# Kernel tuning notes

Measured on AMD Instinct MI355X. Metric: run time of the kernel, lower is better.

Reference implementation:

```python
import jax, jax.numpy as jnp
import numpy as np

N = 2048   # num nodes
D = 512    # hidden_dim


def setup_inputs() -> dict:
    key = jax.random.key(0)
    k1, k2 = jax.random.split(key)
    x = jax.random.normal(k1, (N, D), dtype=jnp.float32)
    # linear: hidden_dim -> 1 (xavier-like scale)
    w = jax.random.normal(k2, (D,), dtype=jnp.float32) * (1.0 / np.sqrt(D))
    b = jnp.zeros((1,), dtype=jnp.float32)
    return {"x": x, "w": w, "b": b}


def reference(x, w, b):
    # euclidean_distance_matrix + linear fused:
    # s[i,j] = sum_d w_d * (x[i,d]-x[j,d])^2 + b
    #        = q_i + q_j - 2*(x*w) @ x^T + b,  q_i = sum_d w_d x[i,d]^2
    xw = x * w                              # [N, D]
    q = jnp.sum(xw * x, axis=1)             # [N]
    cross = xw @ x.T                        # [N, N]
    s = q[:, None] + q[None, :] - 2.0 * cross + b[0]
    grouping_matrix = jax.nn.sigmoid(s)     # [N, N]

    # compute_fielder, similarity_graph='base'
    W = grouping_matrix
    degree = jnp.sum(W, axis=1)
    L = jnp.diag(degree) - W                # symmetric graph Laplacian
    eigen_values, eigen_vectors = jnp.linalg.eigh(L)
    order = jnp.argsort(jnp.abs(eigen_values))
    fielder_value = eigen_values[order[1]]
    fielder_vector = eigen_vectors[:, order[1]]
    return grouping_matrix, fielder_value, fielder_vector
```

## Files before the change

### kernel.cpp

```cpp
#include <hip/hip_runtime.h>
#include <math.h>

constexpr int NN = 2048;
constexpr int DD_ = 512;
constexpr int LM = 64;
constexpr int VS = NN + 32;
constexpr int GPART = 8;
constexpr int MVB = 512;
#define SIGN_FLIP 1


typedef __attribute__((ext_vector_type(4))) float f32x4;
typedef __attribute__((ext_vector_type(8))) short bf16x8;

__device__ inline double waveReduceSum(double v) {
#pragma unroll
  for (int off = 32; off; off >>= 1) v += __shfl_down(v, off, 64);
  return v;
}

__device__ inline double blockReduceSum256(double v) {
  __shared__ double sm[4];
  int lane = threadIdx.x & 63;
  int wid  = threadIdx.x >> 6;
  v = waveReduceSum(v);
  __syncthreads();
  if (lane == 0) sm[wid] = v;
  __syncthreads();
  double r = 0.0;
  if (threadIdx.x < 4) r = sm[threadIdx.x];
  if (wid == 0) {
    r += __shfl_down(r, 2, 64);
    r += __shfl_down(r, 1, 64);
  }
  return r;
}

__device__ inline double blockReduceSum128(double v) {
  __shared__ double sm[2];
  int lane = threadIdx.x & 63;
  int wid  = threadIdx.x >> 6;
  v = waveReduceSum(v);
  if (lane == 0) sm[wid] = v;
  __syncthreads();
  double r = 0.0;
  if (threadIdx.x == 0) r = sm[0] + sm[1];
  return r;
}

__device__ inline unsigned short f2bf(float f) {
  unsigned u = __float_as_uint(f);
  u += 0x7FFFu + ((u >> 16) & 1u);
  return (unsigned short)(u >> 16);
}
__device__ inline float bf2f(unsigned short h) {
  return __uint_as_float(((unsigned)h) << 16);
}

__global__ __launch_bounds__(128) void k_cvtq(const float* __restrict__ x,
                                              const float* __restrict__ w,
                                              float* __restrict__ q,
                                              unsigned short* __restrict__ ah,
                                              unsigned short* __restrict__ al,
                                              unsigned short* __restrict__ bh,
                                              unsigned short* __restrict__ bl) {
  int row = blockIdx.x, t = threadIdx.x;
  int d = 4 * t;
  float4 xv = *(const float4*)&x[(size_t)row * DD_ + d];
  float4 wv = *(const float4*)&w[d];
  float xs[4] = {xv.x, xv.y, xv.z, xv.w};
  float wsv[4] = {wv.x, wv.y, wv.z, wv.w};
  unsigned short rah[4], ral[4], rbh[4], rbl[4];
  float accq = 0.f;
#pragma unroll
  for (int kq = 0; kq < 4; ++kq) {
    float xf = xs[kq], wf = wsv[kq];
    float a = xf * wf;
    unsigned short h = f2bf(a);
    rah[kq] = h;
    ral[kq] = f2bf(a - bf2f(h));
    unsigned short hb = f2bf(xf);
    rbh[kq] = hb;
    rbl[kq] = f2bf(xf - bf2f(hb));
    accq += wf * xf * xf;
  }
  ushort4 vA = {rah[0], rah[1], rah[2], rah[3]};
  ushort4 vAl = {ral[0], ral[1], ral[2], ral[3]};
  ushort4 vB = {rbh[0], rbh[1], rbh[2], rbh[3]};
  ushort4 vBl = {rbl[0], rbl[1], rbl[2], rbl[3]};
  *(ushort4*)&ah[(size_t)row * DD_ + d] = vA;
  *(ushort4*)&al[(size_t)row * DD_ + d] = vAl;
  *(ushort4*)&bh[(size_t)row * DD_ + d] = vB;
  *(ushort4*)&bl[(size_t)row * DD_ + d] = vBl;
  double rq = blockReduceSum128((double)accq);
  if (t == 0) q[row] = (float)rq;
}

__global__ __launch_bounds__(256) void k_Wm(const unsigned short* __restrict__ ah,
                                            const unsigned short* __restrict__ al,
                                            const unsigned short* __restrict__ bh,
                                            const unsigned short* __restrict__ bl,
                                            const float* __restrict__ q,
                                            const float* __restrict__ bptr,
                                            float* __restrict__ out) {
  const int bx = blockIdx.x, by = blockIdx.y;
  if (bx < by) return;
  union SmemU {
    struct { unsigned short As[2][128][40]; unsigned short Bs[2][128][40]; } ab;
    float tr[64][132];
  };
  __shared__ SmemU sm;
  const int t = threadIdx.x;
  const int i0 = by * 128, j0 = bx * 128;
  const int lane = t & 63, wv = t >> 6;
  const int wr = wv >> 1, wc = wv & 1;
  const int fr = lane & 15, kc = lane >> 4;
  const int srow = t >> 1, scol = (t & 1) * 16;

  f32x4 acc[4][4];
#pragma unroll
  for (int a = 0; a < 4; ++a)
#pragma unroll
    for (int b = 0; b < 4; ++b) acc[a][b] = (f32x4){0.f, 0.f, 0.f, 0.f};

  {
    bf16x8 ra0 = *(const bf16x8*)&ah[(size_t)(i0 + srow) * DD_ + scol];
    bf16x8 ra1 = *(const bf16x8*)&ah[(size_t)(i0 + srow) * DD_ + scol + 8];
    bf16x8 rb0 = *(const bf16x8*)&bh[(size_t)(j0 + srow) * DD_ + scol];
    bf16x8 rb1 = *(const bf16x8*)&bh[(size_t)(j0 + srow) * DD_ + scol + 8];
    *(bf16x8*)&sm.ab.As[0][srow][scol] = ra0;
    *(bf16x8*)&sm.ab.As[0][srow][scol + 8] = ra1;
    *(bf16x8*)&sm.ab.Bs[0][srow][scol] = rb0;
    *(bf16x8*)&sm.ab.Bs[0][srow][scol + 8] = rb1;
  }
  __syncthreads();
  int cur = 0;
  for (int s = 0; s < 48; ++s) {
    bf16x8 na0, na1, nb0, nb1;
    if (s + 1 < 48) {
      int pass = (s + 1) >> 4;
      int kk = ((s + 1) & 15) * 32;
      const unsigned short* srcA = (pass == 2) ? al : ah;
      const unsigned short* srcB = (pass == 1) ? bl : bh;
      na0 = *(const bf16x8*)&srcA[(size_t)(i0 + srow) * DD_ + kk + scol];
      na1 = *(const bf16x8*)&srcA[(size_t)(i0 + srow) * DD_ + kk + scol + 8];
      nb0 = *(const bf16x8*)&srcB[(size_t)(j0 + srow) * DD_ + kk + scol];
      nb1 = *(const bf16x8*)&srcB[(size_t)(j0 + srow) * DD_ + kk + scol + 8];
    }
    bf16x8 af[4], bq[4];
#pragma unroll
    for (int a = 0; a < 4; ++a)
      af[a] = *(const bf16x8*)&sm.ab.As[cur][wr * 64 + a * 16 + fr][kc * 8];
#pragma unroll
    for (int b = 0; b < 4; ++b)
      bq[b] = *(const bf16x8*)&sm.ab.Bs[cur][wc * 64 + b * 16 + fr][kc * 8];
#pragma unroll
    for (int a = 0; a < 4; ++a)
#pragma unroll
      for (int b = 0; b < 4; ++b)
        acc[a][b] = __builtin_amdgcn_mfma_f32_16x16x32_bf16(af[a], bq[b], acc[a][b], 0, 0, 0);
    if (s + 1 < 48) {
      *(bf16x8*)&sm.ab.As[cur ^ 1][srow][scol] = na0;
      *(bf16x8*)&sm.ab.As[cur ^ 1][srow][scol + 8] = na1;
      *(bf16x8*)&sm.ab.Bs[cur ^ 1][srow][scol] = nb0;
      *(bf16x8*)&sm.ab.Bs[cur ^ 1][srow][scol + 8] = nb1;
    }
    __syncthreads();
    cur ^= 1;
  }
  float b0 = bptr[0];
#pragma unroll
  for (int a = 0; a < 4; ++a) {
#pragma unroll
    for (int rg = 0; rg < 4; ++rg) {
      int i = i0 + wr * 64 + a * 16 + kc * 4 + rg;
      float qi = q[i];
#pragma unroll
      for (int b = 0; b < 4; ++b) {
        int j = j0 + wc * 64 + b * 16 + fr;
        float s = qi + q[j] - 2.0f * acc[a][b][rg] + b0;
        float sig = 1.0f / (1.0f + expf(-s));
        acc[a][b][rg] = sig;
        out[(size_t)i * NN + j] = sig;
      }
    }
  }
  if (bx != by) {
#pragma unroll
    for (int h = 0; h < 2; ++h) {
      __syncthreads();
      if (wc == h) {
#pragma unroll
        for (int a = 0; a < 4; ++a)
#pragma unroll
          for (int b = 0; b < 4; ++b)
            *(f32x4*)&sm.tr[b * 16 + fr][wr * 64 + a * 16 + kc * 4] = acc[a][b];
      }
      __syncthreads();
#pragma unroll
      for (int p = 0; p < 8; ++p) {
        int f = p * 256 + t;
        int rr_ = f >> 5, c4 = (f & 31) * 4;
        float4 v = *(const float4*)&sm.tr[rr_][c4];
        *(float4*)&out[(size_t)(j0 + h * 64 + rr_) * NN + i0 + c4] = v;
      }
    }
  }
}

__global__ __launch_bounds__(256) void k_init(double* __restrict__ r,
                                              double* __restrict__ part) {
  int t = threadIdx.x;
  double loc[8];
  double s = 0.0;
#pragma unroll
  for (int p = 0; p < 8; ++p) {
    unsigned i = (unsigned)(t + 256 * p);
    unsigned u = i * 2654435761u + 0x9E3779B9u;
    u ^= u >> 16; u *= 0x85EBCA6Bu; u ^= u >> 13; u *= 0xC2B2AE35u; u ^= u >> 16;
    double val = ((double)u / 4294967296.0) - 0.5;
    loc[p] = val; s += val;
  }
  __shared__ double mean_s, inv_s;
  double tot = blockReduceSum256(s);
  if (t == 0) mean_s = tot / (double)NN;
  __syncthreads();
  double mean = mean_s;
  double ss = 0.0;
#pragma unroll
  for (int p = 0; p < 8; ++p) { loc[p] -= mean; ss += loc[p] * loc[p]; }
  double tss = blockReduceSum256(ss);
  if (t == 0) inv_s = 1.0 / sqrt(tss);
  __syncthreads();
  double inv = inv_s;
#pragma unroll
  for (int p = 0; p < 8; ++p) r[t + 256 * p] = loc[p] * inv;
  if (t < GPART) part[t] = (t == 0) ? 1.0 : 0.0;
}

__global__ __launch_bounds__(256) void k_mva(const float* __restrict__ Wm,
                                             double* __restrict__ deg,
                                             const double* __restrict__ rprev,
                                             const double* __restrict__ part,
                                             double* __restrict__ V,
                                             double* __restrict__ wstash,
                                             double* __restrict__ c,
                                             double* __restrict__ beta, int j) {
  int b = blockIdx.x, t = threadIdx.x;
  double ss = 0.0;
#pragma unroll
  for (int p = 0; p < GPART; ++p) ss += part[p];
  double bet = sqrt(ss);
  double inv = (bet > 1e-3) ? 1.0 / bet : 0.0;

  if (b < MVB) {
    const int lane = t & 63, w = t >> 6;
    const int row = b * 4 + w;
    const float* wr = Wm + (size_t)row * NN;
    double acc = 0.0, dsum = 0.0;
    if (j == 0) {
#pragma unroll
      for (int p = 0; p < 8; ++p) {
        int i = 4 * lane + 256 * p;
        float4 wl = *(const float4*)&wr[i];
        dsum += (double)wl.x + (double)wl.y + (double)wl.z + (double)wl.w;
        acc += (double)wl.x * rprev[i] + (double)wl.y * rprev[i + 1] +
               (double)wl.z * rprev[i + 2] + (double)wl.w * rprev[i + 3];
      }
    } else {
#pragma unroll
      for (int p = 0; p < 8; ++p) {
        int i = 4 * lane + 256 * p;
        float4 wl = *(const float4*)&wr[i];
        acc += (double)wl.x * rprev[i] + (double)wl.y * rprev[i + 1] +
               (double)wl.z * rprev[i + 2] + (double)wl.w * rprev[i + 3];
      }
    }
    acc = waveReduceSum(acc);
    if (j == 0) dsum = waveReduceSum(dsum);
    if (lane == 0) {
      double d;
      if (j == 0) { d = dsum; deg[row] = d; }
      else d = deg[row];
      double vj = rprev[row] * inv;
      V[(size_t)j * VS + row] = vj;
      wstash[(size_t)j * VS + row] = d * vj - acc * inv;
      if (row == 0 && j > 0) beta[j - 1] = (bet > 1e-3) ? bet : 0.0;
    }
  } else {
    int q = b - MVB;
    const double* wq = wstash + (size_t)q * VS;
    double a = 0.0;
#pragma unroll
    for (int p = 0; p < 8; ++p) { int i = t + 256 * p; a += wq[i] * rprev[i]; }
    double red = blockReduceSum256(a);
    if (t == 0) c[q] = red * inv;
  }
}

__global__ __launch_bounds__(256) void k_orthb(const double* __restrict__ V,
                                               const double* __restrict__ wstash,
                                               const double* __restrict__ c,
                                               double* __restrict__ r,
                                               double* __restrict__ part,
                                               double* __restrict__ alpha, int j) {
  __shared__ double cs[LM];
  __shared__ double cj_s, s1_s;
  int b = blockIdx.x, t = threadIdx.x;
  const double* wj = wstash + (size_t)j * VS;
  const double* vj = V + (size_t)j * VS;
  double a = 0.0, s = 0.0;
#pragma unroll
  for (int p = 0; p < 8; ++p) {
    int i = t + 256 * p;
    double wv = wj[i];
    a += vj[i] * wv;
    s += wv;
  }
  double cj = blockReduceSum256(a);
  double s1 = blockReduceSum256(s);
  if (t == 0) { cj_s = cj; s1_s = s1; }
  for (int k = t; k < j; k += 256) cs[k] = c[k];
  __syncthreads();
  double cjv = cj_s, s1v = s1_s;
  int i = b * 256 + t;
  double val = wj[i] - s1v / (double)NN - cjv * vj[i];
  for (int k = 0; k < j; ++k) val -= cs[k] * V[(size_t)k * VS + i];
  r[i] = val;
  double rr = blockReduceSum256(val * val);
  if (t == 0) {
    part[b] = rr;
    if (b == 0) alpha[j] = cjv;
  }
}

__device__ inline double guardpiv(double d) {
  if (fabs(d) < 1e-280) return (d < 0.0) ? -1e-280 : 1e-280;
  return d;
}

template <int NB_>
__device__ inline int sturm_cnt(double p, double al_r, double be_r, int nn) {
  const int lim = NB_ ? NB_ : nn;
  int cnt = 0;
  double d = __shfl(al_r, 0, 64) - p;
  if (d < 0.0) cnt++;
  double ai = __shfl(al_r, 1, 64);
  double bi = __shfl(be_r, 0, 64);
  for (int i = 1; i < lim; ++i) {
    double ai_n = 0.0, bi_n = 0.0;
    if (i + 1 < lim) { ai_n = __shfl(al_r, i + 1, 64); bi_n = __shfl(be_r, i, 64); }
    if (fabs(d) < 1e-300) d = (d < 0.0) ? -1e-300 : 1e-300;
    d = (ai - p) - bi * bi / d;
    if (d < 0.0) cnt++;
    ai = ai_n; bi = bi_n;
  }
  return cnt;
}

__global__ __launch_bounds__(64) void k_tri(const double* __restrict__ alpha,
                                            const double* __restrict__ beta,
                                            double* __restrict__ svec) {
  const int t = threadIdx.x;
  double al_r = alpha[t];
  double be_r = (t < LM - 1) ? beta[t] : 0.0;

  int cand = isfinite(al_r) ? LM : t;
  int candb = (t < LM - 1 && (be_r == 0.0 || !isfinite(be_r))) ? (t + 1) : LM;
  int m = min(cand, candb);
#pragma unroll
  for (int off = 32; off; off >>= 1) m = min(m, __shfl_down(m, off, 64));
  m = __shfl(m, 0, 64);
  if (m < 2) m = 2;
  const int n = m;

  double be_prev = __shfl_up(be_r, 1, 64);
  double lo = 1e300, hi = -1e300;
  if (t < n) {
    double rr = 0.0;
    if (t > 0) rr += fabs(be_prev);
    if (t < n - 1) rr += fabs(be_r);
    lo = al_r - rr;
    hi = al_r + rr;
  }
#pragma unroll
  for (int off = 32; off; off >>= 1) {
    lo = fmin(lo, __shfl_down(lo, off, 64));
    hi = fmax(hi, __shfl_down(hi, off, 64));
  }
  lo = __shfl(lo, 0, 64);
  hi = __shfl(hi, 0, 64);

  double B0 = lo, B1 = hi;
  for (int round = 0; round < 3; ++round) {
    double p = B0 + (B1 - B0) * ((double)(t + 1) / 65.0);
    int cnt = (n == LM) ? sturm_cnt<LM>(p, al_r, be_r, n)
                        : sturm_cnt<0>(p, al_r, be_r, n);
    unsigned long long nz = __ballot(cnt > 0);
    double nl, nh;
    if (nz) {
      int first = __ffsll(nz) - 1;
      nh = B0 + (B1 - B0) * ((double)(first + 1) / 65.0);
      nl = (first > 0) ? (B0 + (B1 - B0) * ((double)first / 65.0)) : B0;
    } else {
      nl = B0 + (B1 - B0) * (64.0 / 65.0);
      nh = B1;
    }
    B0 = nl; B1 = nh;
  }
  const double sigma = 0.5 * (B0 + B1);

  double Dgf = 0.0, Dl_s = 0.0, Du_s = 0.0, Du2_s = 0.0;
  int piv_s = 0;
  {
    double dg = __shfl(al_r, 0, 64) - sigma;
    double bl = __shfl(be_r, 0, 64);
    double du = bl;
    double a1 = __shfl(al_r, 1, 64);
    double b1 = (2 < n) ? __shfl(be_r, 1, 64) : 0.0;
    for (int i = 0; i < n - 1; ++i) {
      double a1_n = 0.0, b1_n = 0.0;
      if (i + 2 < n) a1_n = __shfl(al_r, i + 2, 64);
      if (i + 3 < n) b1_n = __shfl(be_r, i + 2, 64);
      double dg_ip1 = a1 - sigma;
      double be_ip1 = b1;
      double dg_n, du_n;
      if (fabs(dg) >= fabs(bl)) {
        double fact = bl / guardpiv(dg);
        if (t == i) { Dgf = dg; Dl_s = fact; Du_s = du; Du2_s = 0.0; piv_s = 0; }
        dg_n = dg_ip1 - fact * du;
        du_n = be_ip1;
      } else {
        double fact = dg / bl;
        if (t == i) { Dgf = bl; Dl_s = fact; Du_s = dg_ip1; Du2_s = be_ip1; piv_s = 1; }
        dg_n = du - fact * dg_ip1;
        du_n = -fact * be_ip1;
      }
      dg = dg_n; du = du_n;
      bl = b1; a1 = a1_n; b1 = b1_n;
    }
    if (t == n - 1) Dgf = dg;
  }

  double bbf = 1.0;
  {
    double cur = 1.0;
    double dl = __shfl(Dl_s, 0, 64);
    int pv = __shfl(piv_s, 0, 64);
    for (int i = 0; i < n - 1; ++i) {
      double dl_n = 0.0; int pv_n = 0;
      if (i + 1 < n - 1) { dl_n = __shfl(Dl_s, i + 1, 64); pv_n = __shfl(piv_s, i + 1, 64); }
      double nxt;
      if (!pv) {
        if (t == i) bbf = cur;
        nxt = 1.0 - dl * cur;
      } else {
        if (t == i) bbf = 1.0;
        nxt = cur - dl;
      }
      cur = nxt;
      dl = dl_n; pv = pv_n;
    }
    if (t == n - 1) bbf = cur;
  }

  double xv = 0.0;
  {
    double idg = 1.0 / guardpiv(Dgf);
    double x1 = 0.0, x2 = 0.0;
    double bi = __shfl(bbf, n - 1, 64);
    double idgi = __shfl(idg, n - 1, 64);
    double dui = __shfl(Du_s, n - 1, 64);
    double du2i = __shfl(Du2_s, n - 1, 64);
    for (int i = n - 1; i >= 0; --i) {
      double bi_n = 0.0, idgi_n = 0.0, dui_n = 0.0, du2i_n = 0.0;
      if (i > 0) {
        bi_n = __shfl(bbf, i - 1, 64);
        idgi_n = __shfl(idg, i - 1, 64);
        dui_n = __shfl(Du_s, i - 1, 64);
        du2i_n = __shfl(Du2_s, i - 1, 64);
      }
      double num = bi;
      if (i < n - 1) num -= dui * x1;
      if (i < n - 2) num -= du2i * x2;
      double xi = num * idgi;
      if (t == i) xv = xi;
      x2 = x1; x1 = xi;
      bi = bi_n; idgi = idgi_n; dui = dui_n; du2i = du2i_n;
    }
  }

  double nrm = (t < n) ? xv * xv : 0.0;
#pragma unroll
  for (int off = 32; off; off >>= 1) nrm += __shfl_down(nrm, off, 64);
  nrm = __shfl(nrm, 0, 64);
  double s = 1.0 / sqrt(nrm);
  svec[t] = (t < n) ? xv * s : 0.0;
}

__global__ __launch_bounds__(256) void k_ritz(const double* __restrict__ V,
                                              const double* __restrict__ s,
                                              double* __restrict__ u) {
  __shared__ double cs[LM];
  int t = threadIdx.x;
  for (int k = t; k < LM; k += 256) cs[k] = s[k];
  __syncthreads();
  int i = blockIdx.x * 256 + t;
  double acc = 0.0;
  for (int k = 0; k < LM; ++k) acc += cs[k] * V[(size_t)k * VS + i];
  u[i] = acc;
}

__global__ __launch_bounds__(256) void k_mvu(const float* __restrict__ Wm,
                                             const double* __restrict__ deg,
                                             const double* __restrict__ v,
                                             double* __restrict__ w) {
  int row = blockIdx.x, t = threadIdx.x;
  const float* wr = Wm + (size_t)row * NN;
  double acc = 0.0;
#pragma unroll
  for (int p = 0; p < 2; ++p) {
    int i = 4 * t + 1024 * p;
    float4 wl = *(const float4*)&wr[i];
    acc += (double)wl.x * v[i] + (double)wl.y * v[i + 1] +
           (double)wl.z * v[i + 2] + (double)wl.w * v[i + 3];
  }
  double r = blockReduceSum256(acc);
  if (t == 0) w[row] = deg[row] * v[row] - r;
}

__global__ __launch_bounds__(256) void k_tail(const double* __restrict__ u,
                                              const double* __restrict__ lu,
                                              float* __restrict__ out_lam,
                                              float* __restrict__ outv) {
  __shared__ double mv[256];
  __shared__ int mi[256];
  __shared__ double mean_s, scale_s;
  int t = threadIdx.x;
  double a = 0.0, b = 0.0;
#pragma unroll
  for (int p = 0; p < 8; ++p) {
    int i = t + 256 * p;
    a += u[i] * lu[i];
    b += u[i] * u[i];
  }
  double ra = blockReduceSum256(a);
  double rb = blockReduceSum256(b);
  if (t == 0) *out_lam = (float)(ra / rb);
  double loc[8];
  double s = 0.0;
#pragma unroll
  for (int p = 0; p < 8; ++p) { loc[p] = u[t + 256 * p]; s += loc[p]; }
  double tot = blockReduceSum256(s);
  if (t == 0) mean_s = tot / (double)NN;
  __syncthreads();
  double mean = mean_s;
  double ss = 0.0, bv = -1.0;
  int bi = 0;
#pragma unroll
  for (int p = 0; p < 8; ++p) {
    loc[p] -= mean;
    ss += loc[p] * loc[p];
    double aa = fabs(loc[p]);
    if (aa > bv) { bv = aa; bi = p; }
  }
  double tss = blockReduceSum256(ss);
  mv[t] = bv; mi[t] = t + 256 * bi;
  __syncthreads();
  for (int off = 128; off; off >>= 1) {
    if (t < off) {
      if (mv[t + off] > mv[t]) { mv[t] = mv[t + off]; mi[t] = mi[t + off]; }
    }
    __syncthreads();
  }
  if (t == 0) {
    int gi = mi[0];
    double best = u[gi] - mean_s;
    double sgn = (best < 0.0) ? -1.0 : 1.0;
#if SIGN_FLIP
    sgn = -sgn;
#endif
    scale_s = sgn / sqrt(tss);
  }
  __syncthreads();
  double sc = scale_s;
#pragma unroll
  for (int p = 0; p < 8; ++p) outv[t + 256 * p] = (float)(loc[p] * sc);
}

extern "C" void kernel_launch(void* const* d_in, const int* in_sizes, int n_in,
                              void* d_out, int out_size, void* d_ws, size_t ws_size,
                              hipStream_t stream) {
  const float* x = (const float*)d_in[0];
  const float* wv = (const float*)d_in[1];
  const float* bp = (const float*)d_in[2];
  float* out = (float*)d_out;

  char* ws = (char*)d_ws;
  size_t off = 0;
  auto alloc = [&](size_t bytes) -> char* {
    char* p = ws + off;
    off = (off + bytes + 255) & ~(size_t)255;
    return p;
  };
  float* q      = (float*)alloc((size_t)NN * 4);
  double* deg   = (double*)alloc((size_t)NN * 8);
  double* r     = (double*)alloc((size_t)NN * 8);
  double* u     = (double*)alloc((size_t)NN * 8);
  double* c     = (double*)alloc((size_t)(LM + 2) * 8);
  double* alpha = (double*)alloc((size_t)LM * 8);
  double* beta  = (double*)alloc((size_t)LM * 8);
  double* svec  = (double*)alloc((size_t)LM * 8);
  double* part  = (double*)alloc((size_t)GPART * 8);
  char* un = alloc((size_t)4 * NN * DD_ * 2);
  unsigned short* ah = (unsigned short*)un;
  unsigned short* al = ah + (size_t)NN * DD_;
  unsigned short* bh = al + (size_t)NN * DD_;
  unsigned short* bl = bh + (size_t)NN * DD_;
  double* V      = (double*)un;
  double* wstash = V + (size_t)LM * VS;
  (void)ws_size; (void)in_sizes; (void)n_in; (void)out_size;

  k_cvtq<<<NN, 128, 0, stream>>>(x, wv, q, ah, al, bh, bl);
  dim3 g(NN / 128, NN / 128);
  k_Wm<<<g, 256, 0, stream>>>(ah, al, bh, bl, q, bp, out);
  k_init<<<1, 256, 0, stream>>>(r, part);

  for (int j = 0; j < LM; ++j) {
    k_mva<<<MVB + j, 256, 0, stream>>>(out, deg, r, part, V, wstash, c, beta, j);
    k_orthb<<<NN / 256, 256, 0, stream>>>(V, wstash, c, r, part, alpha, j);
  }
  k_tri<<<1, 64, 0, stream>>>(alpha, beta, svec);
  k_ritz<<<NN / 256, 256, 0, stream>>>(V, svec, u);
  k_mvu<<<NN, 256, 0, stream>>>(out, deg, u, r);
  k_tail<<<1, 256, 0, stream>>>(u, r, out + (size_t)NN * NN,
                                out + (size_t)NN * NN + 1);
}
```

Before: 810.7 us.

## Fuse Lanczos matvec and orthogonalization kernels using an atomic counter barrier

Each Lanczos step previously ran two kernels: a matvec/projection kernel and then an orthogonalization kernel. They are merged into one launch with 8 extra trailing blocks. Those blocks spin on a per-iteration atomic counter until every matvec and projection block has published its results with relaxed atomic stores and fences, then do the orthogonalization. This halves the number of launches and the inter-kernel gaps in the 64-step loop. In exchange it depends on the trailing blocks being scheduled after the producer blocks, and it adds spin-wait and fence overhead.

```diff
diff --git a/kernel.cpp b/kernel.cpp
--- a/kernel.cpp
+++ b/kernel.cpp
@@ -209,7 +209,8 @@
 }
 
 __global__ __launch_bounds__(256) void k_init(double* __restrict__ r,
-                                              double* __restrict__ part) {
+                                              double* __restrict__ part,
+                                              unsigned* __restrict__ cnt) {
   int t = threadIdx.x;
   double loc[8];
   double s = 0.0;
@@ -236,17 +237,20 @@
 #pragma unroll
   for (int p = 0; p < 8; ++p) r[t + 256 * p] = loc[p] * inv;
   if (t < GPART) part[t] = (t == 0) ? 1.0 : 0.0;
-}
-
-__global__ __launch_bounds__(256) void k_mva(const float* __restrict__ Wm,
-                                             double* __restrict__ deg,
-                                             const double* __restrict__ rprev,
-                                             const double* __restrict__ part,
-                                             double* __restrict__ V,
-                                             double* __restrict__ wstash,
-                                             double* __restrict__ c,
-                                             double* __restrict__ beta, int j) {
-  int b = blockIdx.x, t = threadIdx.x;
+  if (t < LM) cnt[t] = 0;
+}
+
+__global__ __launch_bounds__(256, 4) void k_ab(const float* __restrict__ Wm,
+                                               double* __restrict__ deg,
+                                               double* __restrict__ r,
+                                               double* __restrict__ part,
+                                               double* __restrict__ V,
+                                               double* __restrict__ wstash,
+                                               double* __restrict__ c,
+                                               double* __restrict__ alpha,
+                                               double* __restrict__ beta,
+                                               unsigned* __restrict__ cnt, int j) {
+  const int b = blockIdx.x, t = threadIdx.x;
   double ss = 0.0;
 #pragma unroll
   for (int p = 0; p < GPART; ++p) ss += part[p];
@@ -264,16 +268,16 @@
         int i = 4 * lane + 256 * p;
         float4 wl = *(const float4*)&wr[i];
         dsum += (double)wl.x + (double)wl.y + (double)wl.z + (double)wl.w;
-        acc += (double)wl.x * rprev[i] + (double)wl.y * rprev[i + 1] +
-               (double)wl.z * rprev[i + 2] + (double)wl.w * rprev[i + 3];
+        acc += (double)wl.x * r[i] + (double)wl.y * r[i + 1] +
+               (double)wl.z * r[i + 2] + (double)wl.w * r[i + 3];
       }
     } else {
 #pragma unroll
       for (int p = 0; p < 8; ++p) {
         int i = 4 * lane + 256 * p;
         float4 wl = *(const float4*)&wr[i];
-        acc += (double)wl.x * rprev[i] + (double)wl.y * rprev[i + 1] +
-               (double)wl.z * rprev[i + 2] + (double)wl.w * rprev[i + 3];
+        acc += (double)wl.x * r[i] + (double)wl.y * r[i + 1] +
+               (double)wl.z * r[i + 2] + (double)wl.w * r[i + 3];
       }
     }
     acc = waveReduceSum(acc);
@@ -282,55 +286,63 @@
       double d;
       if (j == 0) { d = dsum; deg[row] = d; }
       else d = deg[row];
-      double vj = rprev[row] * inv;
-      V[(size_t)j * VS + row] = vj;
-      wstash[(size_t)j * VS + row] = d * vj - acc * inv;
+      double vj = r[row] * inv;
+      __hip_atomic_store(&V[(size_t)j * VS + row], vj,
+                         __ATOMIC_RELAXED, __HIP_MEMORY_SCOPE_AGENT);
+      __hip_atomic_store(&wstash[(size_t)j * VS + row], d * vj - acc * inv,
+                         __ATOMIC_RELAXED, __HIP_MEMORY_SCOPE_AGENT);
       if (row == 0 && j > 0) beta[j - 1] = (bet > 1e-3) ? bet : 0.0;
     }
-  } else {
+    __syncthreads();
+    if (t == 0) { __threadfence(); atomicAdd(&cnt[j], 1u); }
+  } else if (b < MVB + j) {
     int q = b - MVB;
     const double* wq = wstash + (size_t)q * VS;
     double a = 0.0;
 #pragma unroll
-    for (int p = 0; p < 8; ++p) { int i = t + 256 * p; a += wq[i] * rprev[i]; }
+    for (int p = 0; p < 8; ++p) { int i = t + 256 * p; a += wq[i] * r[i]; }
     double red = blockReduceSum256(a);
-    if (t == 0) c[q] = red * inv;
-  }
-}
-
-__global__ __launch_bounds__(256) void k_orthb(const double* __restrict__ V,
-                                               const double* __restrict__ wstash,
-                                               const double* __restrict__ c,
-                                               double* __restrict__ r,
-                                               double* __restrict__ part,
-                                               double* __restrict__ alpha, int j) {
-  __shared__ double cs[LM];
-  __shared__ double cj_s, s1_s;
-  int b = blockIdx.x, t = threadIdx.x;
-  const double* wj = wstash + (size_t)j * VS;
-  const double* vj = V + (size_t)j * VS;
-  double a = 0.0, s = 0.0;
-#pragma unroll
-  for (int p = 0; p < 8; ++p) {
-    int i = t + 256 * p;
-    double wv = wj[i];
-    a += vj[i] * wv;
-    s += wv;
-  }
-  double cj = blockReduceSum256(a);
-  double s1 = blockReduceSum256(s);
-  if (t == 0) { cj_s = cj; s1_s = s1; }
-  for (int k = t; k < j; k += 256) cs[k] = c[k];
-  __syncthreads();
-  double cjv = cj_s, s1v = s1_s;
-  int i = b * 256 + t;
-  double val = wj[i] - s1v / (double)NN - cjv * vj[i];
-  for (int k = 0; k < j; ++k) val -= cs[k] * V[(size_t)k * VS + i];
-  r[i] = val;
-  double rr = blockReduceSum256(val * val);
-  if (t == 0) {
-    part[b] = rr;
-    if (b == 0) alpha[j] = cjv;
+    if (t == 0) {
+      __hip_atomic_store(&c[q], red * inv, __ATOMIC_RELAXED, __HIP_MEMORY_SCOPE_AGENT);
+      __threadfence();
+      atomicAdd(&cnt[j], 1u);
+    }
+  } else {
+    const int s = b - MVB - j;
+    __shared__ double cs[LM];
+    __shared__ double cj_s, s1_s;
+    if (t == 0) {
+      const unsigned tgt = (unsigned)(MVB + j);
+      while (__hip_atomic_load(&cnt[j], __ATOMIC_ACQUIRE, __HIP_MEMORY_SCOPE_AGENT) < tgt)
+        __builtin_amdgcn_s_sleep(4);
+    }
+    __syncthreads();
+    __threadfence();
+    const double* wj = wstash + (size_t)j * VS;
+    const double* vj = V + (size_t)j * VS;
+    double a = 0.0, sw = 0.0;
+#pragma unroll
+    for (int p = 0; p < 8; ++p) {
+      int i = t + 256 * p;
+      double wv = wj[i];
+      a += vj[i] * wv;
+      sw += wv;
+    }
+    double cj = blockReduceSum256(a);
+    double s1 = blockReduceSum256(sw);
+    if (t == 0) { cj_s = cj; s1_s = s1; }
+    for (int k = t; k < j; k += 256) cs[k] = c[k];
+    __syncthreads();
+    double cjv = cj_s, s1v = s1_s;
+    int i = s * 256 + t;
+    double val = wj[i] - s1v / (double)NN - cjv * vj[i];
+    for (int k = 0; k < j; ++k) val -= cs[k] * V[(size_t)k * VS + i];
+    r[i] = val;
+    double rr = blockReduceSum256(val * val);
+    if (t == 0) {
+      part[s] = rr;
+      if (s == 0) alpha[j] = cjv;
+    }
   }
 }
 
@@ -612,6 +624,7 @@
   double* beta  = (double*)alloc((size_t)LM * 8);
   double* svec  = (double*)alloc((size_t)LM * 8);
   double* part  = (double*)alloc((size_t)GPART * 8);
+  unsigned* cnt = (unsigned*)alloc((size_t)LM * 4);
   char* un = alloc((size_t)4 * NN * DD_ * 2);
   unsigned short* ah = (unsigned short*)un;
   unsigned short* al = ah + (size_t)NN * DD_;
@@ -624,11 +637,11 @@
   k_cvtq<<<NN, 128, 0, stream>>>(x, wv, q, ah, al, bh, bl);
   dim3 g(NN / 128, NN / 128);
   k_Wm<<<g, 256, 0, stream>>>(ah, al, bh, bl, q, bp, out);
-  k_init<<<1, 256, 0, stream>>>(r, part);
+  k_init<<<1, 256, 0, stream>>>(r, part, cnt);
 
   for (int j = 0; j < LM; ++j) {
-    k_mva<<<MVB + j, 256, 0, stream>>>(out, deg, r, part, V, wstash, c, beta, j);
-    k_orthb<<<NN / 256, 256, 0, stream>>>(V, wstash, c, r, part, alpha, j);
+    k_ab<<<MVB + j + 8, 256, 0, stream>>>(out, deg, r, part, V, wstash, c,
+                                          alpha, beta, cnt, j);
   }
   k_tri<<<1, 64, 0, stream>>>(alpha, beta, svec);
   k_ritz<<<NN / 256, 256, 0, stream>>>(V, svec, u);
```

Measured after the change: 1.454 ms. 1.79x slower.
